# Optimization experiments

Measured on AMD Instinct MI355X. Metric: run time of the kernel, lower is better.

Reference implementation:

```python
import jax, jax.numpy as jnp
import numpy as np

B, S, W = 32, 128, 20
WV, CV = 50000, 128
WD, CE = 300, 50
KS = (2, 3, 4, 5)
NF = 64
TOTF = NF * len(KS)
CF = 300
H = 512
L = 9
LP = L + 2
START, END = L, L + 1
NEG = -10000.0


def setup_inputs():
    key = jax.random.key(0)
    ks = jax.random.split(key, 40)
    def nrm(i, shape, scale=0.1):
        return jax.random.normal(ks[i], shape, dtype=jnp.float32) * scale
    inp = {}
    inp['token_ids'] = jax.random.randint(ks[0], (B, S), 0, WV)
    inp['char_ids'] = jax.random.randint(ks[1], (B, S, W), 0, CV)
    lens = jnp.sort(jax.random.randint(ks[2], (B,), S // 2, S + 1))[::-1]
    inp['lens'] = lens.astype(jnp.int32)
    inp['labels'] = jax.random.randint(ks[3], (B, S), 0, L)
    inp['word_embed'] = nrm(4, (WV, WD))
    inp['char_embed'] = nrm(5, (CV, CE))
    for j, k in enumerate(KS):
        inp['conv_w%d' % k] = nrm(6 + j, (k, CE, NF))
        inp['conv_b%d' % k] = nrm(10 + j, (NF,))
    inp['ff_w'] = nrm(14, (CF, TOTF))
    inp['ff_b'] = nrm(15, (CF,))
    inp['wgate_w'] = nrm(16, (WD, WD))
    inp['cgate_w'] = nrm(17, (CF, CF))
    inp['gate_w'] = nrm(18, (WD, WD))
    inp['wih_f'] = nrm(19, (4 * H, WD))
    inp['whh_f'] = nrm(20, (4 * H, H))
    inp['b_f'] = nrm(21, (4 * H,))
    inp['wih_b'] = nrm(22, (4 * H, WD))
    inp['whh_b'] = nrm(23, (4 * H, H))
    inp['b_b'] = nrm(24, (4 * H,))
    inp['out_w'] = nrm(25, (L, 2 * H))
    inp['out_b'] = nrm(26, (L,))
    inp['trn'] = nrm(27, (LP, LP))
    return inp


def _char_cnn(char_ids, char_embed, convs):
    x = char_embed[char_ids.reshape(-1, W)]  # [B*S, W, CE]
    feats = []
    for w, b in convs:
        y = jax.lax.conv_general_dilated(x, w, (1,), 'VALID',
                                         dimension_numbers=('NWC', 'WIO', 'NWC')) + b
        feats.append(jnp.max(jax.nn.relu(y), axis=1))  # max over time -> [B*S, NF]
    return jnp.concatenate(feats, axis=1)  # [B*S, TOTF]


def _run_lstm(x, mask, wih, whh, b, reverse):
    # x [B,S,D], mask bool [B,S]; padded steps freeze state and emit zeros (packed-seq semantics)
    xg = jnp.einsum('bsd,gd->bsg', x, wih) + b  # [B,S,4H]
    xg_t = jnp.swapaxes(xg, 0, 1)               # [S,B,4H]
    m_t = jnp.swapaxes(mask, 0, 1)[..., None]   # [S,B,1]
    h0 = jnp.zeros((x.shape[0], H), x.dtype)
    def step(carry, inp):
        h, c = carry
        g_t, m = inp
        g = g_t + h @ whh.T
        i, f, gg, o = jnp.split(g, 4, axis=-1)  # torch gate order i,f,g,o
        cn = jax.nn.sigmoid(f) * c + jax.nn.sigmoid(i) * jnp.tanh(gg)
        hn = jax.nn.sigmoid(o) * jnp.tanh(cn)
        h = jnp.where(m, hn, h)
        c = jnp.where(m, cn, c)
        return (h, c), jnp.where(m, hn, 0.0)
    _, out = jax.lax.scan(step, (h0, h0), (xg_t, m_t), reverse=reverse)
    return jnp.swapaxes(out, 0, 1)  # [B,S,H]


def _crf_norm(logits, mask, trn):
    # logits [B,S,LP]; trn[i,j] = score(prev=j -> next=i)
    alpha = logits[:, 0] + trn[:, START][None, :]
    lt = jnp.swapaxes(logits, 0, 1)[1:]                 # [S-1,B,LP]
    mt = jnp.swapaxes(mask, 0, 1)[1:][..., None]        # [S-1,B,1]
    def step(alpha, inp):
        lg, m = inp
        new = jax.scipy.special.logsumexp(alpha[:, None, :] + trn[None], axis=2) + lg
        return jnp.where(m, new, alpha), None
    alpha, _ = jax.lax.scan(step, alpha, (lt, mt))
    return jax.scipy.special.logsumexp(alpha + trn[END][None, :], axis=1)


def _crf_gold(logits, labels, lens, mask, trn):
    fm = mask.astype(logits.dtype)
    emit = jnp.take_along_axis(logits, labels[..., None], axis=2)[..., 0]
    emit = jnp.sum(emit * fm, axis=1)
    trans = trn[labels[:, 1:], labels[:, :-1]] * fm[:, 1:]
    first = trn[labels[:, 0], START]
    last_lab = jnp.take_along_axis(labels, (lens - 1)[:, None], axis=1)[:, 0]
    return emit + jnp.sum(trans, axis=1) + first + trn[END, last_lab]


def reference(token_ids, char_ids, lens, labels, word_embed, char_embed,
              conv_w2, conv_b2, conv_w3, conv_b3, conv_w4, conv_b4, conv_w5, conv_b5,
              ff_w, ff_b, wgate_w, cgate_w, gate_w,
              wih_f, whh_f, b_f, wih_b, whh_b, b_b, out_w, out_b, trn):
    word_in = word_embed[token_ids]                               # [B,S,WD]
    convs = [(conv_w2, conv_b2), (conv_w3, conv_b3), (conv_w4, conv_b4), (conv_w5, conv_b5)]
    ch = _char_cnn(char_ids, char_embed, convs)                   # [B*S,TOTF]
    char_in = (ch @ ff_w.T + ff_b).reshape(B, S, CF)              # CharCNNFF output
    g = jax.nn.sigmoid(jnp.tanh(word_in @ wgate_w.T + char_in @ cgate_w.T) @ gate_w.T)
    feats = g * word_in + (1.0 - g) * char_in                     # gated fusion (dropout = eval identity)
    mask = jnp.arange(S)[None, :] < lens[:, None]                 # [B,S] bool
    hf = _run_lstm(feats, mask, wih_f, whh_f, b_f, False)
    hb = _run_lstm(feats, mask, wih_b, whh_b, b_b, True)
    lstm_out = jnp.concatenate([hf, hb], axis=-1)                 # [B,S,2H]
    logits = lstm_out @ out_w.T + out_b                           # [B,S,L]
    pads = jnp.full((B, S, 2), NEG, logits.dtype)
    logits = jnp.concatenate([logits, pads], axis=2)              # pad_logits -> [B,S,LP]
    norm = _crf_norm(logits, mask, trn)
    gold = _crf_gold(logits, labels, lens, mask, trn)
    loglik = gold - norm
    return (loglik, logits)
```

## Files before the change

### kernel.cpp

```cpp
#include <hip/hip_runtime.h>

#define NB    32
#define SEQ   128
#define WCH   20
#define CED   50
#define NFLT  64
#define WDIM  300
#define HD    512
#define NWORD 4096
#define LPAD  11
#define NEGV  -10000.0f
#define LSTM_BLOCKS 16

typedef float f32x4 __attribute__((ext_vector_type(4)));
typedef float f32x16 __attribute__((ext_vector_type(16)));
typedef __bf16 bf16x8 __attribute__((ext_vector_type(8)));
typedef unsigned short u16x8 __attribute__((ext_vector_type(8)));
typedef unsigned short u16x4 __attribute__((ext_vector_type(4)));
typedef unsigned long long ull;

static __device__ __forceinline__ unsigned short f2bf(float f) {
  unsigned u = __builtin_bit_cast(unsigned, f);
  u += 0x7fffu + ((u >> 16) & 1u);
  return (unsigned short)(u >> 16);
}
static __device__ __forceinline__ float bf2f(unsigned short s) {
  unsigned u = ((unsigned)s) << 16;
  return __builtin_bit_cast(float, u);
}
static __device__ __forceinline__ float sigf(float x) { return 1.0f / (1.0f + expf(-x)); }

__global__ void cvt_kernel(const float* __restrict__ src, unsigned short* __restrict__ dst, int n4)
{
  int i = blockIdx.x * 256 + threadIdx.x;
  if (i < n4) {
    f32x4 v = *(const f32x4*)&src[i * 4];
    u16x4 o;
    #pragma unroll
    for (int j = 0; j < 4; j++) o[j] = f2bf(v[j]);
    *(u16x4*)&dst[i * 4] = o;
  }
}

__global__ __launch_bounds__(256) void conv_kernel(
    const int* __restrict__ char_ids, const float* __restrict__ char_embed,
    const float* __restrict__ w2, const float* __restrict__ b2,
    const float* __restrict__ w3, const float* __restrict__ b3,
    const float* __restrict__ w4, const float* __restrict__ b4,
    const float* __restrict__ w5, const float* __restrict__ b5,
    unsigned short* __restrict__ ch)
{
  __shared__ __align__(16) float xT[CED][WCH];
  int wi = blockIdx.x;
  int tid = threadIdx.x;
  for (int e = tid; e < WCH * CED; e += 256) {
    int p = e / CED, c = e - p * CED;
    int cid = char_ids[wi * WCH + p];
    xT[c][p] = char_embed[cid * CED + c];
  }
  __syncthreads();
  int w = tid >> 6, f = tid & 63;
  int k = w + 2;
  int P = WCH - k + 1;
  const float* cw = (w == 0) ? w2 : (w == 1) ? w3 : (w == 2) ? w4 : w5;
  const float* cb = (w == 0) ? b2 : (w == 1) ? b3 : (w == 2) ? b4 : b5;
  float acc[19];
  #pragma unroll
  for (int p = 0; p < 19; p++) acc[p] = 0.f;
  for (int c = 0; c < CED; c++) {
    float xr[20];
    const float4* rowp = (const float4*)&xT[c][0];
    #pragma unroll
    for (int q = 0; q < 5; q++) {
      float4 v = rowp[q];
      xr[4*q+0] = v.x; xr[4*q+1] = v.y; xr[4*q+2] = v.z; xr[4*q+3] = v.w;
    }
    #pragma unroll
    for (int dw = 0; dw < 5; dw++) {
      if (dw < k) {
        float wv = cw[(dw * CED + c) * NFLT + f];
        #pragma unroll
        for (int p = 0; p < 19; p++) {
          if (p < P) acc[p] += xr[p + dw] * wv;
        }
      }
    }
  }
  float m = acc[0];
  #pragma unroll
  for (int p = 1; p < 19; p++) if (p < P) m = fmaxf(m, acc[p]);
  ch[wi * 256 + w * 64 + f] = f2bf(fmaxf(0.f, m + cb[f]));
}

__global__ void gather_word_kernel(const int* __restrict__ token_ids,
                                   const float* __restrict__ word_embed,
                                   unsigned short* __restrict__ word_in)
{
  int idx = blockIdx.x * 256 + threadIdx.x;
  if (idx < NWORD * WDIM) {
    int i = idx / WDIM, c = idx - i * WDIM;
    word_in[idx] = f2bf(word_embed[token_ids[i] * WDIM + c]);
  }
}

__global__ __launch_bounds__(512) void gemm2_kernel(
    const unsigned short* __restrict__ A1, const unsigned short* __restrict__ A2,
    const unsigned short* __restrict__ B1, const unsigned short* __restrict__ B2,
    const float* __restrict__ bias, unsigned short* __restrict__ Cbf,
    int M, int N, int K1, int K2, int act, int gridN)
{
  const int Kt = K1 + K2;
  __shared__ __align__(16) unsigned short As[256 * 40];
  __shared__ __align__(16) unsigned short Bs[128 * 40];
  int bid = blockIdx.x;
  int tm = bid / gridN, tn = bid - tm * gridN;
  int m0 = tm * 256, n0 = tn * 128;
  int tid = threadIdx.x;
  int lane = tid & 63, w = tid >> 6;
  int wr = (w >> 1) * 64, wc = (w & 1) * 64;
  f32x4 acc[4][4] = {};
  int fr = lane & 15, fk = (lane >> 4) * 8;

  for (int k0 = 0; k0 < Kt; k0 += 32) {
    __syncthreads();
    #pragma unroll
    for (int i = 0; i < 4; i++) {
      int q = tid + i * 512;
      int r = q >> 3, c4 = q & 7;
      int kx = k0 + c4 * 4;
      int ra = m0 + r;
      u16x4 v = {0, 0, 0, 0};
      if (kx < Kt && ra < M) {
        v = (kx < K1) ? *(const u16x4*)&A1[(size_t)ra * K1 + kx]
                      : *(const u16x4*)&A2[(size_t)ra * K2 + (kx - K1)];
      }
      *(u16x4*)&As[r * 40 + c4 * 4] = v;
    }
    #pragma unroll
    for (int i = 0; i < 2; i++) {
      int q = tid + i * 512;
      int r = q >> 3, c4 = q & 7;
      int kx = k0 + c4 * 4;
      int rb = n0 + r;
      u16x4 v = {0, 0, 0, 0};
      if (kx < Kt && rb < N) {
        v = (kx < K1) ? *(const u16x4*)&B1[(size_t)rb * K1 + kx]
                      : *(const u16x4*)&B2[(size_t)rb * K2 + (kx - K1)];
      }
      *(u16x4*)&Bs[r * 40 + c4 * 4] = v;
    }
    __syncthreads();
    bf16x8 a[4], b[4];
    #pragma unroll
    for (int mt = 0; mt < 4; mt++)
      a[mt] = *(const bf16x8*)&As[(wr + mt * 16 + fr) * 40 + fk];
    #pragma unroll
    for (int nt = 0; nt < 4; nt++)
      b[nt] = *(const bf16x8*)&Bs[(wc + nt * 16 + fr) * 40 + fk];
    #pragma unroll
    for (int mt = 0; mt < 4; mt++)
      #pragma unroll
      for (int nt = 0; nt < 4; nt++)
        acc[mt][nt] = __builtin_amdgcn_mfma_f32_16x16x32_bf16(a[mt], b[nt], acc[mt][nt], 0, 0, 0);
  }

  #pragma unroll
  for (int mt = 0; mt < 4; mt++) {
    #pragma unroll
    for (int nt = 0; nt < 4; nt++) {
      #pragma unroll
      for (int j = 0; j < 4; j++) {
        int row = m0 + wr + mt * 16 + (lane >> 4) * 4 + j;
        int col = n0 + wc + nt * 16 + (lane & 15);
        if (row < M && col < N) {
          float v = acc[mt][nt][j];
          if (bias) v += bias[col];
          if (act == 1)      v = tanhf(v);
          else if (act == 2) v = sigf(v);
          Cbf[(size_t)row * N + col] = f2bf(v);
        }
      }
    }
  }
}

__global__ void feats_kernel(const unsigned short* __restrict__ g,
                             const unsigned short* __restrict__ word_in,
                             const unsigned short* __restrict__ char_in,
                             unsigned short* __restrict__ feats,
                             unsigned* __restrict__ flags)
{
  if (blockIdx.x == 0 && threadIdx.x < 32)
    __hip_atomic_store(&flags[threadIdx.x], 0u, __ATOMIC_RELAXED, __HIP_MEMORY_SCOPE_AGENT);
  int idx = blockIdx.x * 256 + threadIdx.x;
  if (idx < NWORD * WDIM) {
    float gg = bf2f(g[idx]);
    feats[idx] = f2bf(gg * bf2f(word_in[idx]) + (1.f - gg) * bf2f(char_in[idx]));
  }
}

__global__ __launch_bounds__(512, 2) void lstm_kernel(
    const unsigned short* __restrict__ xg_f, const unsigned short* __restrict__ xg_b,
    const float* __restrict__ whh_f, const float* __restrict__ whh_b,
    const int* __restrict__ lens,
    float* __restrict__ lstm_out, unsigned short* __restrict__ h_glob,
    unsigned* __restrict__ flags)
{
  int bid = blockIdx.x;
  int dir = bid >> 3, sl = bid & 7;
  int hs0 = sl << 6;
  int tid = threadIdx.x, lane = tid & 63, w = tid >> 6;
  int g = w & 3, hc = w >> 2;
  int l31 = lane & 31, le = lane >> 5;
  const unsigned short* xg = dir ? xg_b : xg_f;
  const float* whh = dir ? whh_b : whh_f;
  unsigned short* hg = h_glob + dir * (2 * NB * HD);
  unsigned* myflags = flags + dir * 16;

  bf16x8 wf[32];
  {
    const float* src = whh + (size_t)(g * HD + hs0 + hc * 32 + l31) * HD + le * 8;
    #pragma unroll
    for (int kk = 0; kk < 32; kk++) {
      u16x8 tv;
      #pragma unroll
      for (int j = 0; j < 8; j++) tv[j] = f2bf(src[kk * 16 + j]);
      wf[kk] = __builtin_bit_cast(bf16x8, tv);
    }
  }

  __shared__ __align__(16) unsigned short hS[16384];
  __shared__ float Gs[NB][260];

  int b = tid >> 4;
  int u = (tid & 15) << 2;
  int srow = tid >> 4, sq = tid & 15;
  int mylen = lens[b];
  float c4[4] = {0.f,0.f,0.f,0.f}, hp4[4] = {0.f,0.f,0.f,0.f};

  ull xq0, xq1, xq2, xq3;
  {
    int t0 = dir ? (SEQ - 1) : 0;
    const ull* xp = (const ull*)&xg[((size_t)(b * SEQ + t0)) * 2048 + hs0 + u];
    xq0 = xp[0]; xq1 = xp[128]; xq2 = xp[256]; xq3 = xp[384];
  }

  for (int s = 0; s < SEQ; s++) {
    int t = dir ? (SEQ - 1 - s) : s;
    f32x16 acc0 = {}, acc1 = {};

    if (s > 0) {
      if (w == 0) {
        unsigned tgt = (unsigned)s;
        for (;;) {
          unsigned v = (lane < 8)
            ? __hip_atomic_load(&myflags[lane], __ATOMIC_RELAXED, __HIP_MEMORY_SCOPE_AGENT)
            : tgt;
          if (__all(v >= tgt)) break;
          __builtin_amdgcn_s_sleep(1);
        }
      }
      __syncthreads();
      {
        const ull* hq = (const ull*)(hg + (s & 1) * (NB * HD));
        ull v[8];
        #pragma unroll
        for (int i = 0; i < 8; i++)
          v[i] = __hip_atomic_load(hq + srow * 128 + sq * 8 + i, __ATOMIC_RELAXED, __HIP_MEMORY_SCOPE_AGENT);
        int rs = ((srow ^ (sq & 7)) & 31) << 4;
        #pragma unroll
        for (int e2 = 0; e2 < 4; e2++) {
          int kk = 2 * sq + (e2 >> 1), e = e2 & 1;
          uint4 qv;
          qv.x = (unsigned)v[2*e2];     qv.y = (unsigned)(v[2*e2] >> 32);
          qv.z = (unsigned)v[2*e2+1];   qv.w = (unsigned)(v[2*e2+1] >> 32);
          *(uint4*)((char*)hS + (((kk * 2 + e) << 9) + rs)) = qv;
        }
      }
      __syncthreads();
      #pragma unroll
      for (int kk = 0; kk < 32; kk += 2) {
        int rs = ((l31 ^ ((kk >> 1) & 7)) & 31) << 4;
        int a0off = ((kk * 2 + le) << 9) + rs;
        int a1off = ((kk * 2 + 2 + le) << 9) + rs;
        bf16x8 a0 = *(const bf16x8*)((const char*)hS + a0off);
        bf16x8 a1 = *(const bf16x8*)((const char*)hS + a1off);
        acc0 = __builtin_amdgcn_mfma_f32_32x32x16_bf16(a0, wf[kk], acc0, 0, 0, 0);
        acc1 = __builtin_amdgcn_mfma_f32_32x32x16_bf16(a1, wf[kk+1], acc1, 0, 0, 0);
      }
    }

    #pragma unroll
    for (int r = 0; r < 16; r++) {
      int bb = (r & 3) + 8 * (r >> 2) + 4 * le;
      Gs[bb][g * 64 + hc * 32 + l31] = acc0[r] + acc1[r];
    }
    __syncthreads();

    f32x4 gi  = *(const f32x4*)&Gs[b][u];
    f32x4 gfv = *(const f32x4*)&Gs[b][64 + u];
    f32x4 ggv = *(const f32x4*)&Gs[b][128 + u];
    f32x4 gov = *(const f32x4*)&Gs[b][192 + u];
    bool mk = (t < mylen);
    f32x4 outv;
    ull hpk = 0;
    #pragma unroll
    for (int j = 0; j < 4; j++) {
      float xi = bf2f((unsigned short)(xq0 >> (16*j)));
      float xf = bf2f((unsigned short)(xq1 >> (16*j)));
      float xG = bf2f((unsigned short)(xq2 >> (16*j)));
      float xo = bf2f((unsigned short)(xq3 >> (16*j)));
      float iv = sigf(xi + gi[j]);
      float fv = sigf(xf + gfv[j]);
      float Gv = tanhf(xG + ggv[j]);
      float ov = sigf(xo + gov[j]);
      float cn = fv * c4[j] + iv * Gv;
      float hn = ov * tanhf(cn);
      if (mk) c4[j] = cn;
      float hk = mk ? hn : hp4[j];
      hp4[j] = hk;
      outv[j] = mk ? hn : 0.f;
      hpk |= ((ull)f2bf(hk)) << (16*j);
    }
    {
      ull* hd = (ull*)(hg + ((s & 1) ^ 1) * (NB * HD));
      __hip_atomic_store(&hd[(b * HD + hs0 + u) >> 2], hpk, __ATOMIC_RELAXED, __HIP_MEMORY_SCOPE_AGENT);
    }

    __syncthreads();
    if (tid == 0)
      __hip_atomic_store(&myflags[sl], (unsigned)(s + 1), __ATOMIC_RELAXED, __HIP_MEMORY_SCOPE_AGENT);

    size_t obase = ((size_t)(b * SEQ + t)) * 1024 + dir * HD + hs0 + u;
    *(f32x4*)&lstm_out[obase] = outv;
    if (s + 1 < SEQ) {
      int tn = dir ? (SEQ - 2 - s) : (s + 1);
      const ull* xp = (const ull*)&xg[((size_t)(b * SEQ + tn)) * 2048 + hs0 + u];
      xq0 = xp[0]; xq1 = xp[128]; xq2 = xp[256]; xq3 = xp[384];
    }
  }
}

__global__ __launch_bounds__(64) void logits_kernel(
    const float* __restrict__ lstm_out, const float* __restrict__ out_w,
    const float* __restrict__ out_b, float* __restrict__ lg)
{
  int rw = blockIdx.x, j = threadIdx.x;
  const float* row = lstm_out + (size_t)rw * 1024;
  float s[9];
  #pragma unroll
  for (int l = 0; l < 9; l++) s[l] = 0.f;
  for (int e = j; e < 1024; e += 64) {
    float x = row[e];
    #pragma unroll
    for (int l = 0; l < 9; l++) s[l] += x * out_w[l * 1024 + e];
  }
  #pragma unroll
  for (int l = 0; l < 9; l++) {
    #pragma unroll
    for (int off = 32; off > 0; off >>= 1) s[l] += __shfl_xor(s[l], off);
  }
  float v = NEGV;
  if (j < 9) {
    float r = (j==0)?s[0]:(j==1)?s[1]:(j==2)?s[2]:(j==3)?s[3]:(j==4)?s[4]:
              (j==5)?s[5]:(j==6)?s[6]:(j==7)?s[7]:s[8];
    v = r + out_b[j];
  }
  if (j < LPAD) lg[(size_t)rw * LPAD + j] = v;
}

__global__ __launch_bounds__(64) void crf_gold_kernel(
    const float* __restrict__ lg, const int* __restrict__ labels,
    const int* __restrict__ lens, const float* __restrict__ trn, float* __restrict__ gold)
{
  int b = blockIdx.x, j = threadIdx.x;
  int len = lens[b];
  const int* lab = labels + b * SEQ;
  const float* l0 = lg + (size_t)b * SEQ * LPAD;
  float s = 0.f;
  for (int t = j; t < SEQ; t += 64) {
    if (t < len) {
      s += l0[t * LPAD + lab[t]];
      if (t >= 1) s += trn[lab[t] * LPAD + lab[t - 1]];
    }
  }
  #pragma unroll
  for (int off = 32; off > 0; off >>= 1) s += __shfl_xor(s, off);
  if (j == 0) {
    s += trn[lab[0] * LPAD + 9];
    s += trn[10 * LPAD + lab[len - 1]];
    gold[b] = s;
  }
}

__global__ __launch_bounds__(64) void crf_norm_kernel(
    const float* __restrict__ lg, const int* __restrict__ lens,
    const float* __restrict__ trn, const float* __restrict__ gold, float* __restrict__ out_ll)
{
  int b = blockIdx.x, i = threadIdx.x;
  int len = lens[b];
  const float* l0 = lg + (size_t)b * SEQ * LPAD;
  bool act = (i < LPAD);
  float trow[LPAD];
  #pragma unroll
  for (int jj = 0; jj < LPAD; jj++) trow[jj] = act ? trn[i * LPAD + jj] : 0.f;
  float alpha = act ? (l0[i] + trow[9]) : -1e30f;

  for (int t = 1; t < SEQ; t++) {
    float vj[LPAD];
    #pragma unroll
    for (int jj = 0; jj < LPAD; jj++) vj[jj] = __shfl(alpha, jj) + trow[jj];
    float mx = vj[0];
    #pragma unroll
    for (int jj = 1; jj < LPAD; jj++) mx = fmaxf(mx, vj[jj]);
    float sum = 0.f;
    #pragma unroll
    for (int jj = 0; jj < LPAD; jj++) sum += expf(vj[jj] - mx);
    float lgv = act ? l0[t * LPAD + i] : 0.f;
    float nw = mx + logf(sum) + lgv;
    if (act && t < len) alpha = nw;
  }
  float vj[LPAD];
  #pragma unroll
  for (int jj = 0; jj < LPAD; jj++) vj[jj] = __shfl(alpha, jj) + trn[10 * LPAD + jj];
  float mx = vj[0];
  #pragma unroll
  for (int jj = 1; jj < LPAD; jj++) mx = fmaxf(mx, vj[jj]);
  float sum = 0.f;
  #pragma unroll
  for (int jj = 0; jj < LPAD; jj++) sum += expf(vj[jj] - mx);
  if (i == 0) out_ll[b] = gold[b] - (mx + logf(sum));
}

extern "C" void kernel_launch(void* const* d_in, const int* in_sizes, int n_in,
                              void* d_out, int out_size, void* d_ws, size_t ws_size,
                              hipStream_t stream)
{
  (void)in_sizes; (void)n_in; (void)out_size; (void)ws_size;
  const int*   token_ids = (const int*)d_in[0];
  const int*   char_ids  = (const int*)d_in[1];
  const int*   lens      = (const int*)d_in[2];
  const int*   labels    = (const int*)d_in[3];
  const float* word_embed= (const float*)d_in[4];
  const float* char_embed= (const float*)d_in[5];
  const float* w2 = (const float*)d_in[6];  const float* cb2 = (const float*)d_in[7];
  const float* w3 = (const float*)d_in[8];  const float* cb3 = (const float*)d_in[9];
  const float* w4 = (const float*)d_in[10]; const float* cb4 = (const float*)d_in[11];
  const float* w5 = (const float*)d_in[12]; const float* cb5 = (const float*)d_in[13];
  const float* ff_w = (const float*)d_in[14]; const float* ff_b = (const float*)d_in[15];
  const float* wgate_w = (const float*)d_in[16];
  const float* cgate_w = (const float*)d_in[17];
  const float* gate_w  = (const float*)d_in[18];
  const float* wih_f = (const float*)d_in[19]; const float* whh_f = (const float*)d_in[20];
  const float* b_f   = (const float*)d_in[21];
  const float* wih_b = (const float*)d_in[22]; const float* whh_b = (const float*)d_in[23];
  const float* b_b   = (const float*)d_in[24];
  const float* out_w = (const float*)d_in[25]; const float* out_b = (const float*)d_in[26];
  const float* trn   = (const float*)d_in[27];

  char* ws = (char*)d_ws;
  size_t off = 0;
  auto alloc = [&](size_t bytes) { void* p = ws + off; off += (bytes + 255) & ~(size_t)255; return p; };
  unsigned short* ch_bf    = (unsigned short*)alloc((size_t)NWORD * 256 * 2);
  unsigned short* word_bf  = (unsigned short*)alloc((size_t)NWORD * WDIM * 2);
  unsigned short* char_bf  = (unsigned short*)alloc((size_t)NWORD * WDIM * 2);
  unsigned short* t1_bf    = (unsigned short*)alloc((size_t)NWORD * WDIM * 2);
  unsigned short* g_bf     = (unsigned short*)alloc((size_t)NWORD * WDIM * 2);
  unsigned short* feats_bf = (unsigned short*)alloc((size_t)NWORD * WDIM * 2);
  unsigned short* ffw_bf   = (unsigned short*)alloc((size_t)300 * 256 * 2);
  unsigned short* wgw_bf   = (unsigned short*)alloc((size_t)300 * 300 * 2);
  unsigned short* cgw_bf   = (unsigned short*)alloc((size_t)300 * 300 * 2);
  unsigned short* gw_bf    = (unsigned short*)alloc((size_t)300 * 300 * 2);
  unsigned short* wihf_bf  = (unsigned short*)alloc((size_t)2048 * 300 * 2);
  unsigned short* wihb_bf  = (unsigned short*)alloc((size_t)2048 * 300 * 2);
  unsigned short* xgf = (unsigned short*)alloc((size_t)NWORD * 2048 * 2);
  unsigned short* xgb = (unsigned short*)alloc((size_t)NWORD * 2048 * 2);
  float* lstm_o   = (float*)alloc((size_t)NWORD * 1024 * 4);
  unsigned short* hglob = (unsigned short*)alloc((size_t)2 * 2 * NB * HD * 2);
  float* gold     = (float*)alloc((size_t)NB * 4);
  unsigned* flags = (unsigned*)alloc(256);

  float* outp   = (float*)d_out;
  float* loglik = outp;
  float* logits = outp + NB;

  conv_kernel<<<NWORD, 256, 0, stream>>>(char_ids, char_embed, w2, cb2, w3, cb3, w4, cb4, w5, cb5, ch_bf);
  gather_word_kernel<<<(NWORD * WDIM + 255) / 256, 256, 0, stream>>>(token_ids, word_embed, word_bf);
  cvt_kernel<<<(300*256/4 + 255)/256, 256, 0, stream>>>(ff_w, ffw_bf, 300*256/4);
  cvt_kernel<<<(300*300/4 + 255)/256, 256, 0, stream>>>(wgate_w, wgw_bf, 300*300/4);
  cvt_kernel<<<(300*300/4 + 255)/256, 256, 0, stream>>>(cgate_w, cgw_bf, 300*300/4);
  cvt_kernel<<<(300*300/4 + 255)/256, 256, 0, stream>>>(gate_w, gw_bf, 300*300/4);
  cvt_kernel<<<(2048*300/4 + 255)/256, 256, 0, stream>>>(wih_f, wihf_bf, 2048*300/4);
  cvt_kernel<<<(2048*300/4 + 255)/256, 256, 0, stream>>>(wih_b, wihb_bf, 2048*300/4);
  gemm2_kernel<<<16 * 3, 512, 0, stream>>>(ch_bf, ch_bf, ffw_bf, ffw_bf, ff_b, char_bf,
                                           NWORD, 300, 256, 0, 0, 3);
  gemm2_kernel<<<16 * 3, 512, 0, stream>>>(word_bf, char_bf, wgw_bf, cgw_bf, nullptr, t1_bf,
                                           NWORD, 300, 300, 300, 1, 3);
  gemm2_kernel<<<16 * 3, 512, 0, stream>>>(t1_bf, t1_bf, gw_bf, gw_bf, nullptr, g_bf,
                                           NWORD, 300, 300, 0, 2, 3);
  feats_kernel<<<(NWORD * WDIM + 255) / 256, 256, 0, stream>>>(g_bf, word_bf, char_bf, feats_bf, flags);
  gemm2_kernel<<<16 * 16, 512, 0, stream>>>(feats_bf, feats_bf, wihf_bf, wihf_bf, b_f, xgf,
                                            NWORD, 2048, 300, 0, 0, 16);
  gemm2_kernel<<<16 * 16, 512, 0, stream>>>(feats_bf, feats_bf, wihb_bf, wihb_bf, b_b, xgb,
                                            NWORD, 2048, 300, 0, 0, 16);
  {
    void* args[] = { (void*)&xgf, (void*)&xgb, (void*)&whh_f, (void*)&whh_b,
                     (void*)&lens, (void*)&lstm_o, (void*)&hglob, (void*)&flags };
    hipLaunchCooperativeKernel((void*)lstm_kernel, dim3(LSTM_BLOCKS), dim3(512), args, 0, stream);
  }
  logits_kernel<<<NWORD, 64, 0, stream>>>(lstm_o, out_w, out_b, logits);
  crf_gold_kernel<<<NB, 64, 0, stream>>>(logits, labels, lens, trn, gold);
  crf_norm_kernel<<<NB, 64, 0, stream>>>(logits, lens, trn, gold, loglik);
}
```

Baseline: 1.293 ms.

## Stage conv weights in LDS, batch words per block, merge cvt and CRF kernels

```diff
diff --git a/kernel.cpp b/kernel.cpp
--- a/kernel.cpp
+++ b/kernel.cpp
@@ -11,6 +11,7 @@
 #define LPAD  11
 #define NEGV  -10000.0f
 #define LSTM_BLOCKS 16
+#define CONV_WPB 16
 
 typedef float f32x4 __attribute__((ext_vector_type(4)));
 typedef float f32x16 __attribute__((ext_vector_type(16)));
@@ -30,16 +31,27 @@
 }
 static __device__ __forceinline__ float sigf(float x) { return 1.0f / (1.0f + expf(-x)); }
 
-__global__ void cvt_kernel(const float* __restrict__ src, unsigned short* __restrict__ dst, int n4)
+__global__ void cvt6_kernel(const float* __restrict__ s0, unsigned short* __restrict__ d0,
+                            const float* __restrict__ s1, unsigned short* __restrict__ d1,
+                            const float* __restrict__ s2, unsigned short* __restrict__ d2,
+                            const float* __restrict__ s3, unsigned short* __restrict__ d3,
+                            const float* __restrict__ s4, unsigned short* __restrict__ d4,
+                            const float* __restrict__ s5, unsigned short* __restrict__ d5)
 {
   int i = blockIdx.x * 256 + threadIdx.x;
-  if (i < n4) {
-    f32x4 v = *(const f32x4*)&src[i * 4];
-    u16x4 o;
-    #pragma unroll
-    for (int j = 0; j < 4; j++) o[j] = f2bf(v[j]);
-    *(u16x4*)&dst[i * 4] = o;
-  }
+  const float* src; unsigned short* dst; int k;
+  if      (i < 19200)  { src = s0; dst = d0; k = i; }
+  else if (i < 41700)  { src = s1; dst = d1; k = i - 19200; }
+  else if (i < 64200)  { src = s2; dst = d2; k = i - 41700; }
+  else if (i < 86700)  { src = s3; dst = d3; k = i - 64200; }
+  else if (i < 240300) { src = s4; dst = d4; k = i - 86700; }
+  else if (i < 393900) { src = s5; dst = d5; k = i - 240300; }
+  else return;
+  f32x4 v = *(const f32x4*)&src[k * 4];
+  u16x4 o;
+  #pragma unroll
+  for (int j = 0; j < 4; j++) o[j] = f2bf(v[j]);
+  *(u16x4*)&dst[k * 4] = o;
 }
 
 __global__ __launch_bounds__(256) void conv_kernel(
@@ -50,46 +62,64 @@
     const float* __restrict__ w5, const float* __restrict__ b5,
     unsigned short* __restrict__ ch)
 {
+  __shared__ __align__(16) unsigned short wS[44800];
   __shared__ __align__(16) float xT[CED][WCH];
-  int wi = blockIdx.x;
+  __shared__ int idsS[WCH];
   int tid = threadIdx.x;
-  for (int e = tid; e < WCH * CED; e += 256) {
-    int p = e / CED, c = e - p * CED;
-    int cid = char_ids[wi * WCH + p];
-    xT[c][p] = char_embed[cid * CED + c];
-  }
-  __syncthreads();
   int w = tid >> 6, f = tid & 63;
   int k = w + 2;
   int P = WCH - k + 1;
-  const float* cw = (w == 0) ? w2 : (w == 1) ? w3 : (w == 2) ? w4 : w5;
+
+  for (int e = tid; e < 44800; e += 256) {
+    float v;
+    if      (e < 6400)  v = w2[e];
+    else if (e < 16000) v = w3[e - 6400];
+    else if (e < 28800) v = w4[e - 16000];
+    else                v = w5[e - 28800];
+    wS[e] = f2bf(v);
+  }
+  const int offs = (w == 0) ? 0 : (w == 1) ? 6400 : (w == 2) ? 16000 : 28800;
   const float* cb = (w == 0) ? b2 : (w == 1) ? b3 : (w == 2) ? b4 : b5;
-  float acc[19];
-  #pragma unroll
-  for (int p = 0; p < 19; p++) acc[p] = 0.f;
-  for (int c = 0; c < CED; c++) {
-    float xr[20];
-    const float4* rowp = (const float4*)&xT[c][0];
-    #pragma unroll
-    for (int q = 0; q < 5; q++) {
-      float4 v = rowp[q];
-      xr[4*q+0] = v.x; xr[4*q+1] = v.y; xr[4*q+2] = v.z; xr[4*q+3] = v.w;
-    }
-    #pragma unroll
-    for (int dw = 0; dw < 5; dw++) {
-      if (dw < k) {
-        float wv = cw[(dw * CED + c) * NFLT + f];
-        #pragma unroll
-        for (int p = 0; p < 19; p++) {
-          if (p < P) acc[p] += xr[p + dw] * wv;
+  float cbv = cb[f];
+
+  for (int i = 0; i < CONV_WPB; i++) {
+    int wi = blockIdx.x * CONV_WPB + i;
+    __syncthreads();
+    if (tid < WCH) idsS[tid] = char_ids[wi * WCH + tid];
+    __syncthreads();
+    for (int e = tid; e < WCH * CED; e += 256) {
+      int p = e / CED, c = e - p * CED;
+      xT[c][p] = char_embed[idsS[p] * CED + c];
+    }
+    __syncthreads();
+
+    float acc[19];
+    #pragma unroll
+    for (int p = 0; p < 19; p++) acc[p] = 0.f;
+    for (int c = 0; c < CED; c++) {
+      float xr[20];
+      const float4* rowp = (const float4*)&xT[c][0];
+      #pragma unroll
+      for (int q = 0; q < 5; q++) {
+        float4 v = rowp[q];
+        xr[4*q+0] = v.x; xr[4*q+1] = v.y; xr[4*q+2] = v.z; xr[4*q+3] = v.w;
+      }
+      #pragma unroll
+      for (int dw = 0; dw < 5; dw++) {
+        if (dw < k) {
+          float wv = bf2f(wS[offs + (dw * CED + c) * NFLT + f]);
+          #pragma unroll
+          for (int p = 0; p < 19; p++) {
+            if (p < P) acc[p] += xr[p + dw] * wv;
+          }
         }
       }
     }
-  }
-  float m = acc[0];
-  #pragma unroll
-  for (int p = 1; p < 19; p++) if (p < P) m = fmaxf(m, acc[p]);
-  ch[wi * 256 + w * 64 + f] = f2bf(fmaxf(0.f, m + cb[f]));
+    float m = acc[0];
+    #pragma unroll
+    for (int p = 1; p < 19; p++) if (p < P) m = fmaxf(m, acc[p]);
+    ch[wi * 256 + w * 64 + f] = f2bf(fmaxf(0.f, m + cbv));
+  }
 }
 
 __global__ void gather_word_kernel(const int* __restrict__ token_ids,
@@ -369,37 +399,27 @@
   if (j < LPAD) lg[(size_t)rw * LPAD + j] = v;
 }
 
-__global__ __launch_bounds__(64) void crf_gold_kernel(
+__global__ __launch_bounds__(64) void crf_kernel(
     const float* __restrict__ lg, const int* __restrict__ labels,
-    const int* __restrict__ lens, const float* __restrict__ trn, float* __restrict__ gold)
-{
-  int b = blockIdx.x, j = threadIdx.x;
+    const int* __restrict__ lens, const float* __restrict__ trn, float* __restrict__ out_ll)
+{
+  int b = blockIdx.x, i = threadIdx.x;
   int len = lens[b];
   const int* lab = labels + b * SEQ;
   const float* l0 = lg + (size_t)b * SEQ * LPAD;
-  float s = 0.f;
-  for (int t = j; t < SEQ; t += 64) {
+
+  float gs = 0.f;
+  for (int t = i; t < SEQ; t += 64) {
     if (t < len) {
-      s += l0[t * LPAD + lab[t]];
-      if (t >= 1) s += trn[lab[t] * LPAD + lab[t - 1]];
-    }
-  }
-  #pragma unroll
-  for (int off = 32; off > 0; off >>= 1) s += __shfl_xor(s, off);
-  if (j == 0) {
-    s += trn[lab[0] * LPAD + 9];
-    s += trn[10 * LPAD + lab[len - 1]];
-    gold[b] = s;
-  }
-}
-
-__global__ __launch_bounds__(64) void crf_norm_kernel(
-    const float* __restrict__ lg, const int* __restrict__ lens,
-    const float* __restrict__ trn, const float* __restrict__ gold, float* __restrict__ out_ll)
-{
-  int b = blockIdx.x, i = threadIdx.x;
-  int len = lens[b];
-  const float* l0 = lg + (size_t)b * SEQ * LPAD;
+      gs += l0[t * LPAD + lab[t]];
+      if (t >= 1) gs += trn[lab[t] * LPAD + lab[t - 1]];
+    }
+  }
+  #pragma unroll
+  for (int off = 32; off > 0; off >>= 1) gs += __shfl_xor(gs, off);
+  gs += trn[lab[0] * LPAD + 9];
+  gs += trn[10 * LPAD + lab[len - 1]];
+
   bool act = (i < LPAD);
   float trow[LPAD];
   #pragma unroll
@@ -429,7 +449,7 @@
   float sum = 0.f;
   #pragma unroll
   for (int jj = 0; jj < LPAD; jj++) sum += expf(vj[jj] - mx);
-  if (i == 0) out_ll[b] = gold[b] - (mx + logf(sum));
+  if (i == 0) out_ll[b] = gs - (mx + logf(sum));
 }
 
 extern "C" void kernel_launch(void* const* d_in, const int* in_sizes, int n_in,
@@ -477,21 +497,16 @@
   unsigned short* xgb = (unsigned short*)alloc((size_t)NWORD * 2048 * 2);
   float* lstm_o   = (float*)alloc((size_t)NWORD * 1024 * 4);
   unsigned short* hglob = (unsigned short*)alloc((size_t)2 * 2 * NB * HD * 2);
-  float* gold     = (float*)alloc((size_t)NB * 4);
   unsigned* flags = (unsigned*)alloc(256);
 
   float* outp   = (float*)d_out;
   float* loglik = outp;
   float* logits = outp + NB;
 
-  conv_kernel<<<NWORD, 256, 0, stream>>>(char_ids, char_embed, w2, cb2, w3, cb3, w4, cb4, w5, cb5, ch_bf);
+  conv_kernel<<<NWORD / CONV_WPB, 256, 0, stream>>>(char_ids, char_embed, w2, cb2, w3, cb3, w4, cb4, w5, cb5, ch_bf);
   gather_word_kernel<<<(NWORD * WDIM + 255) / 256, 256, 0, stream>>>(token_ids, word_embed, word_bf);
-  cvt_kernel<<<(300*256/4 + 255)/256, 256, 0, stream>>>(ff_w, ffw_bf, 300*256/4);
-  cvt_kernel<<<(300*300/4 + 255)/256, 256, 0, stream>>>(wgate_w, wgw_bf, 300*300/4);
-  cvt_kernel<<<(300*300/4 + 255)/256, 256, 0, stream>>>(cgate_w, cgw_bf, 300*300/4);
-  cvt_kernel<<<(300*300/4 + 255)/256, 256, 0, stream>>>(gate_w, gw_bf, 300*300/4);
-  cvt_kernel<<<(2048*300/4 + 255)/256, 256, 0, stream>>>(wih_f, wihf_bf, 2048*300/4);
-  cvt_kernel<<<(2048*300/4 + 255)/256, 256, 0, stream>>>(wih_b, wihb_bf, 2048*300/4);
+  cvt6_kernel<<<(393900 + 255) / 256, 256, 0, stream>>>(ff_w, ffw_bf, wgate_w, wgw_bf, cgate_w, cgw_bf,
+                                                        gate_w, gw_bf, wih_f, wihf_bf, wih_b, wihb_bf);
   gemm2_kernel<<<16 * 3, 512, 0, stream>>>(ch_bf, ch_bf, ffw_bf, ffw_bf, ff_b, char_bf,
                                            NWORD, 300, 256, 0, 0, 3);
   gemm2_kernel<<<16 * 3, 512, 0, stream>>>(word_bf, char_bf, wgw_bf, cgw_bf, nullptr, t1_bf,
@@ -509,6 +524,5 @@
     hipLaunchCooperativeKernel((void*)lstm_kernel, dim3(LSTM_BLOCKS), dim3(512), args, 0, stream);
   }
   logits_kernel<<<NWORD, 64, 0, stream>>>(lstm_o, out_w, out_b, logits);
-  crf_gold_kernel<<<NB, 64, 0, stream>>>(logits, labels, lens, trn, gold);
-  crf_norm_kernel<<<NB, 64, 0, stream>>>(logits, lens, trn, gold, loglik);
-}
+  crf_kernel<<<NB, 64, 0, stream>>>(logits, labels, lens, trn, loglik);
+}
```

Result: slower. 1.558 ms (+20.5%).
